# Performance work log

Measured on AMD Instinct MI355X. Metric: run time of the kernel, lower is better.

The kernel has to match this reference:

```python
import jax, jax.numpy as jnp
import numpy as np

D_MODEL = 1024
N_HEADS = 16
HEAD_DIM = D_MODEL // N_HEADS  # 64


def setup_inputs() -> dict:
    key = jax.random.key(0)
    k1, k2, k3 = jax.random.split(key, 3)
    x = jax.random.normal(k1, (2, 2048, D_MODEL), dtype=jnp.float32)
    # nn.Linear(d, 3d, bias=False): store transposed so y = x @ W
    w_qkv = jax.random.normal(k2, (D_MODEL, 3 * D_MODEL), dtype=jnp.float32) * (D_MODEL ** -0.5)
    w_proj = jax.random.normal(k3, (D_MODEL, D_MODEL), dtype=jnp.float32) * (D_MODEL ** -0.5)
    return {"x": x, "w_qkv": w_qkv, "w_proj": w_proj}


def reference(x, w_qkv, w_proj):
    b, n, _ = x.shape
    qkv = x @ w_qkv  # [b, n, 3*d_model]
    # einops 'b n (h d qkv) -> qkv b h n d': qkv axis is innermost of the split
    qkv = qkv.reshape(b, n, N_HEADS, HEAD_DIM, 3)
    q = jnp.moveaxis(qkv[..., 0], 1, 2)  # [b, h, n, d]
    k = jnp.moveaxis(qkv[..., 1], 1, 2)
    v = jnp.moveaxis(qkv[..., 2], 1, 2)
    scale = HEAD_DIM ** -0.5
    scores = jnp.einsum('bhqd,bhkd->bhqk', q, k) * scale  # [b, h, n, n]
    causal = jnp.tril(jnp.ones((n, n), dtype=bool))
    scores = jnp.where(causal[None, None], scores, -jnp.inf)
    attn = jax.nn.softmax(scores, axis=-1)
    out = jnp.einsum('bhqk,bhkd->bhqd', attn, v)  # [b, h, n, d]
    out = jnp.moveaxis(out, 1, 2).reshape(b, n, D_MODEL)  # 'b h n d -> b n (h d)'
    return out @ w_proj
```

## Files before the change

kernel.cpp:

```cpp
#include <hip/hip_runtime.h>
#include <cstdint>
#include <cstddef>

#define D_MODEL 1024
#define N_HEADS 16
#define HEAD_DIM 64
#define SEQ 2048
#define BATCH 2

typedef __attribute__((ext_vector_type(8))) short bf16x8;
typedef __attribute__((ext_vector_type(4))) float f32x4;

__device__ inline unsigned short f2bf(float f) {
    union { float f; unsigned u; } v; v.f = f;
    unsigned r = v.u + 0x7fffu + ((v.u >> 16) & 1u);
    return (unsigned short)(r >> 16);
}

__device__ __forceinline__ void gload_lds16(const unsigned short* g, unsigned short* l) {
    __builtin_amdgcn_global_load_lds(
        (const __attribute__((address_space(1))) unsigned int*)g,
        (__attribute__((address_space(3))) unsigned int*)l, 16, 0, 0);
}

#define WAITCNT_VM4 0x0F74
#define WAITCNT_VM0 0x0F70

__global__ __launch_bounds__(256) void fused_convert_kernel(
    const float* __restrict__ X, unsigned short* __restrict__ Xb,
    const float* __restrict__ Wq, unsigned short* __restrict__ Wqt,
    const float* __restrict__ Wp, unsigned short* __restrict__ Wpt)
{
    const int blk = blockIdx.x;
    const int tid = threadIdx.x;
    __shared__ float t[32][33];

    if (blk < 2048) {
        const int idx = blk * 256 + tid;
        const float4* src = (const float4*)X;
        float4 v0 = src[idx * 2], v1 = src[idx * 2 + 1];
        union { unsigned short u[8]; uint4 v; } o;
        o.u[0] = f2bf(v0.x); o.u[1] = f2bf(v0.y); o.u[2] = f2bf(v0.z); o.u[3] = f2bf(v0.w);
        o.u[4] = f2bf(v1.x); o.u[5] = f2bf(v1.y); o.u[6] = f2bf(v1.z); o.u[7] = f2bf(v1.w);
        ((uint4*)Xb)[idx] = o.v;
    } else if (blk < 5120) {
        const int bb = blk - 2048;
        const int c0 = (bb % 96) * 32, r0 = (bb / 96) * 32;
        const int a = tid & 31, b = tid >> 5;
#pragma unroll
        for (int i = 0; i < 32; i += 8)
            t[b + i][a] = Wq[(size_t)(r0 + b + i) * (3 * D_MODEL) + c0 + a];
        __syncthreads();
#pragma unroll
        for (int i = 0; i < 32; i += 8) {
            const int c = c0 + b + i;
            const int np = (c % 3) * 1024 + c / 3;
            Wqt[(size_t)np * D_MODEL + r0 + a] = f2bf(t[a][b + i]);
        }
    } else {
        const int bb = blk - 5120;
        const int c0 = (bb % 32) * 32, r0 = (bb / 32) * 32;
        const int a = tid & 31, b = tid >> 5;
#pragma unroll
        for (int i = 0; i < 32; i += 8)
            t[b + i][a] = Wp[(size_t)(r0 + b + i) * D_MODEL + c0 + a];
        __syncthreads();
#pragma unroll
        for (int i = 0; i < 32; i += 8)
            Wpt[(size_t)(c0 + b + i) * D_MODEL + r0 + a] = f2bf(t[a][b + i]);
    }
}

__global__ __launch_bounds__(256) void v_transpose(
    const unsigned short* __restrict__ V, unsigned short* __restrict__ Vt)
{
    const int n0 = blockIdx.x * 64;
    const int bh = blockIdx.y;
    __shared__ unsigned short t[64 * 72];
    const int tid = threadIdx.x;
    const uint4* src = (const uint4*)(V + ((size_t)bh * SEQ + n0) * HEAD_DIM);
#pragma unroll
    for (int it = 0; it < 2; it++) {
        const int lin = tid + it * 256;
        const int row = lin >> 3, p = lin & 7;
        ((uint4*)t)[row * 9 + p] = src[lin];
    }
    __syncthreads();
#pragma unroll
    for (int it = 0; it < 2; it++) {
        const int lin = tid + it * 256;
        const int drow = lin >> 3, p = lin & 7;
        union { unsigned short u[8]; uint4 v; } o;
#pragma unroll
        for (int e = 0; e < 8; e++) o.u[e] = t[(p * 8 + e) * 72 + drow];
        ((uint4*)(Vt + ((size_t)bh * HEAD_DIM + drow) * SEQ + n0))[p] = o.v;
    }
}

#define GEMM_PIPE3_BODY(A_, B_, KBASE, NITER)                                  \
    const int tid = threadIdx.x;                                               \
    const int w = tid >> 6, lane = tid & 63;                                   \
    const int l15 = lane & 15, quad = lane >> 4;                               \
    const int wr = w >> 1, wc = w & 1;                                         \
    const int row0 = blockIdx.y * 128, col0 = blockIdx.x * 128;                \
    __shared__ unsigned short As[3][4096];                                     \
    __shared__ unsigned short Bs[3][4096];                                     \
    const f32x4 zero4 = {0.f, 0.f, 0.f, 0.f};                                  \
    f32x4 acc[4][4];                                                           \
    _Pragma("unroll") for (int i = 0; i < 4; i++)                              \
        _Pragma("unroll") for (int j = 0; j < 4; j++) acc[i][j] = zero4;       \
    auto stage_ = [&](int sb_, int kt_) {                                      \
        const int k0 = (KBASE) + kt_ * 32 + quad * 8;                          \
        _Pragma("unroll") for (int i = 0; i < 2; i++) {                        \
            const int f = w * 2 + i;                                           \
            gload_lds16((A_) + (size_t)(row0 + f * 16 + l15) * D_MODEL + k0,   \
                        &As[sb_][f * 512 + lane * 8]);                         \
            gload_lds16((B_) + (size_t)(col0 + f * 16 + l15) * D_MODEL + k0,   \
                        &Bs[sb_][f * 512 + lane * 8]);                         \
        }                                                                      \
    };                                                                         \
    stage_(0, 0);                                                              \
    stage_(1, 1);                                                              \
    int sb = 0;                                                                \
    for (int kt = 0; kt < (NITER); kt++) {                                     \
        if (kt < (NITER) - 1) {                                                \
            __builtin_amdgcn_s_waitcnt(WAITCNT_VM4);                           \
            __builtin_amdgcn_s_barrier();                                      \
            if (kt + 2 < (NITER)) stage_((sb + 2 > 2) ? sb - 1 : sb + 2, kt + 2); \
        } else {                                                               \
            __builtin_amdgcn_s_waitcnt(WAITCNT_VM0);                           \
            __builtin_amdgcn_s_barrier();                                      \
        }                                                                      \
        bf16x8 af[4], bfr[4];                                                  \
        _Pragma("unroll") for (int i = 0; i < 4; i++)                          \
            af[i] = *(const bf16x8*)&As[sb][(wr * 4 + i) * 512 + lane * 8];    \
        _Pragma("unroll") for (int j = 0; j < 4; j++)                          \
            bfr[j] = *(const bf16x8*)&Bs[sb][(wc * 4 + j) * 512 + lane * 8];   \
        _Pragma("unroll") for (int i = 0; i < 4; i++)                          \
            _Pragma("unroll") for (int j = 0; j < 4; j++)                      \
                acc[i][j] = __builtin_amdgcn_mfma_f32_16x16x32_bf16(           \
                    af[i], bfr[j], acc[i][j], 0, 0, 0);                        \
        sb = (sb == 2) ? 0 : sb + 1;                                           \
    }

__global__ __launch_bounds__(256) void gemm_qkv_mfma(
    const unsigned short* __restrict__ A, const unsigned short* __restrict__ B,
    unsigned short* __restrict__ Q, unsigned short* __restrict__ Kq,
    unsigned short* __restrict__ Vb)
{
    GEMM_PIPE3_BODY(A, B, 0, 32)
    const int nbase = col0 + wc * 64;
    const int which = nbase >> 10;
    unsigned short* const dst = (which == 0) ? Q : (which == 1) ? Kq : Vb;
    const float oscale = (which == 0) ? 0.125f : 1.0f;
#pragma unroll
    for (int i = 0; i < 4; i++) {
#pragma unroll
        for (int r = 0; r < 4; r++) {
            const int row = row0 + wr * 64 + i * 16 + quad * 4 + r;
            const int bb = row >> 11, n = row & (SEQ - 1);
#pragma unroll
            for (int j = 0; j < 4; j++) {
                const int idx = (nbase + j * 16 + l15) & 1023;
                const int h = idx >> 6, dd = idx & 63;
                dst[(((size_t)(bb * N_HEADS + h)) * SEQ + n) * HEAD_DIM + dd] =
                    f2bf(acc[i][j][r] * oscale);
            }
        }
    }
}

__global__ __launch_bounds__(256) void gemm_proj_splitk(
    const unsigned short* __restrict__ A, const unsigned short* __restrict__ B,
    float* __restrict__ P)
{
    const int kbase = blockIdx.z * 512;
    GEMM_PIPE3_BODY(A, B, kbase, 16)
    float* const dst = P + (size_t)blockIdx.z * (4096ull * 1024ull);
#pragma unroll
    for (int i = 0; i < 4; i++) {
#pragma unroll
        for (int r = 0; r < 4; r++) {
            const int row = row0 + wr * 64 + i * 16 + quad * 4 + r;
#pragma unroll
            for (int j = 0; j < 4; j++) {
                const int c = col0 + wc * 64 + j * 16 + l15;
                dst[(size_t)row * D_MODEL + c] = acc[i][j][r];
            }
        }
    }
}

__global__ __launch_bounds__(256) void add_out_kernel(
    const float* __restrict__ P, float* __restrict__ out)
{
    const float4* p0 = (const float4*)P;
    const float4* p1 = (const float4*)(P + 4096ull * 1024ull);
    float4* o = (float4*)out;
    const int base = (blockIdx.x * 256 + threadIdx.x) * 4;
#pragma unroll
    for (int j = 0; j < 4; j++) {
        float4 a = p0[base + j], b = p1[base + j];
        float4 r = {a.x + b.x, a.y + b.y, a.z + b.z, a.w + b.w};
        o[base + j] = r;
    }
}

__global__ __launch_bounds__(256) void flash_attn_kernel(
    const unsigned short* __restrict__ Q,
    const unsigned short* __restrict__ K,
    const unsigned short* __restrict__ Vt,
    unsigned short* __restrict__ O)
{
    const int idx = blockIdx.x;
    const int bh = idx & 31;
    const int qt2 = idx >> 5;
    const int hi = qt2 >> 3, lo = qt2 & 7;
    const int qt = (hi == 0) ? lo : (hi == 1) ? 31 - lo : (hi == 2) ? lo + 8 : 23 - lo;

    const int tid = threadIdx.x;
    const int w = tid >> 6, lane = tid & 63;
    const int l15 = lane & 15, quad = lane >> 4;

    __shared__ unsigned short Ks[2][4096];
    __shared__ unsigned short Vs[2][4096];
    __shared__ unsigned short Ps[4][1024];

    bf16x8 qf[2];
    {
        const unsigned short* qrow =
            Q + ((size_t)bh * SEQ + qt * 64 + w * 16 + l15) * HEAD_DIM;
        qf[0] = *(const bf16x8*)(qrow + quad * 8);
        qf[1] = *(const bf16x8*)(qrow + 32 + quad * 8);
    }

    const f32x4 zero4 = {0.f, 0.f, 0.f, 0.f};
    f32x4 o_acc[4] = {zero4, zero4, zero4, zero4};
    float m_i = -1e30f, l_i = 0.f;

    auto stage = [&](int bf, int kt_t) {
        const int key0 = kt_t * 64;
#pragma unroll
        for (int i = 0; i < 2; i++) {
            const int f = w * 2 + i;
            const int ct = f >> 1, kh = f & 1;
            gload_lds16(K + ((size_t)bh * SEQ + key0 + ct * 16 + l15) * HEAD_DIM
                          + kh * 32 + quad * 8,
                        &Ks[bf][f * 512 + lane * 8]);
            gload_lds16(Vt + ((size_t)bh * HEAD_DIM + ct * 16 + l15) * SEQ
                           + key0 + kh * 32 + quad * 8,
                        &Vs[bf][f * 512 + lane * 8]);
        }
    };

    stage(0, 0);
    int buf = 0;

    const int qg = qt * 64 + w * 16 + l15;

    for (int kt = 0; kt <= qt; kt++) {
        __syncthreads();
        if (kt < qt) stage(buf ^ 1, kt + 1);

        f32x4 st[4] = {zero4, zero4, zero4, zero4};
#pragma unroll
        for (int kh = 0; kh < 2; kh++) {
#pragma unroll
            for (int ct = 0; ct < 4; ct++) {
                bf16x8 kf = *(const bf16x8*)&Ks[buf][(ct * 2 + kh) * 512 + lane * 8];
                st[ct] = __builtin_amdgcn_mfma_f32_16x16x32_bf16(kf, qf[kh], st[ct], 0, 0, 0);
            }
        }

        const bool diag = (kt == qt);
        float mt = -1e30f;
#pragma unroll
        for (int ct = 0; ct < 4; ct++) {
#pragma unroll
            for (int r = 0; r < 4; r++) {
                float v = st[ct][r];
                const int kg = kt * 64 + ct * 16 + quad * 4 + r;
                if (diag && kg > qg) v = -1e30f;
                st[ct][r] = v;
                mt = fmaxf(mt, v);
            }
        }
        mt = fmaxf(mt, __shfl_xor(mt, 16));
        mt = fmaxf(mt, __shfl_xor(mt, 32));

        const float mn = fmaxf(m_i, mt);
        const float alpha = __expf(m_i - mn);
        m_i = mn;

        float ls = 0.f;
#pragma unroll
        for (int ct = 0; ct < 4; ct++) {
            union { unsigned short u[4]; uint2 v; } pk;
#pragma unroll
            for (int r = 0; r < 4; r++) {
                float p = __expf(st[ct][r] - mn);
                ls += p;
                pk.u[r] = f2bf(p);
            }
            const int addr = (ct >> 1) * 512 + ((ct & 1) * 2 + (quad >> 1)) * 128
                           + l15 * 8 + (quad & 1) * 4;
            *(uint2*)&Ps[w][addr] = pk.v;
        }
        ls += __shfl_xor(ls, 16);
        ls += __shfl_xor(ls, 32);
        l_i = l_i * alpha + ls;

        float ar[4];
#pragma unroll
        for (int r = 0; r < 4; r++)
            ar[r] = __shfl(alpha, (lane & 48) | (quad * 4 + r));
#pragma unroll
        for (int dt = 0; dt < 4; dt++)
#pragma unroll
            for (int r = 0; r < 4; r++)
                o_acc[dt][r] *= ar[r];

#pragma unroll
        for (int kh = 0; kh < 2; kh++) {
            bf16x8 pa = *(const bf16x8*)&Ps[w][kh * 512 + quad * 128 + l15 * 8];
#pragma unroll
            for (int dt = 0; dt < 4; dt++) {
                bf16x8 vf = *(const bf16x8*)&Vs[buf][(dt * 2 + kh) * 512 + lane * 8];
                o_acc[dt] = __builtin_amdgcn_mfma_f32_16x16x32_bf16(pa, vf, o_acc[dt], 0, 0, 0);
            }
        }
        buf ^= 1;
    }

    const float linv = 1.0f / l_i;
    float lr[4];
#pragma unroll
    for (int r = 0; r < 4; r++)
        lr[r] = __shfl(linv, (lane & 48) | (quad * 4 + r));

    const int b = bh >> 4, h = bh & 15;
#pragma unroll
    for (int r = 0; r < 4; r++) {
        const int q = qt * 64 + w * 16 + quad * 4 + r;
        unsigned short* orow = O + ((size_t)b * SEQ + q) * D_MODEL + h * HEAD_DIM;
#pragma unroll
        for (int dt = 0; dt < 4; dt++)
            orow[dt * 16 + l15] = f2bf(o_acc[dt][r] * lr[r]);
    }
}

extern "C" void kernel_launch(void* const* d_in, const int* in_sizes, int n_in,
                              void* d_out, int out_size, void* d_ws, size_t ws_size,
                              hipStream_t stream) {
    const float* x      = (const float*)d_in[0];
    const float* w_qkv  = (const float*)d_in[1];
    const float* w_proj = (const float*)d_in[2];
    float* out = (float*)d_out;

    unsigned short* Xb  = (unsigned short*)d_ws;
    unsigned short* Wqt = Xb  + (size_t)4 * 1024 * 1024;
    unsigned short* Wpt = Wqt + (size_t)3 * 1024 * 1024;
    unsigned short* Qb  = Wpt + (size_t)1 * 1024 * 1024;
    unsigned short* Kb  = Qb  + (size_t)4 * 1024 * 1024;
    unsigned short* Vb  = Kb  + (size_t)4 * 1024 * 1024;
    unsigned short* Vtb = Vb  + (size_t)4 * 1024 * 1024;
    unsigned short* Ob  = Vtb + (size_t)4 * 1024 * 1024;

    float* Pp = (float*)Qb;

    fused_convert_kernel<<<dim3(6144), 256, 0, stream>>>(
        x, Xb, w_qkv, Wqt, w_proj, Wpt);

    gemm_qkv_mfma<<<dim3(3 * D_MODEL / 128, BATCH * SEQ / 128), 256, 0, stream>>>(
        Xb, Wqt, Qb, Kb, Vb);

    v_transpose<<<dim3(SEQ / 64, BATCH * N_HEADS), 256, 0, stream>>>(Vb, Vtb);

    flash_attn_kernel<<<dim3(SEQ / 64 * BATCH * N_HEADS), 256, 0, stream>>>(
        Qb, Kb, Vtb, Ob);

    gemm_proj_splitk<<<dim3(D_MODEL / 128, BATCH * SEQ / 128, 2), 256, 0, stream>>>(
        Ob, Wpt, Pp);

    add_out_kernel<<<dim3(1024), 256, 0, stream>>>(Pp, out);
}
```

Measured before the change: 222.0 us.

## Use hardware bf16 packing, fold Q scale into weights, lazy softmax rescale, setprio

Replaces software bf16 rounding with the packed v_cvt_pk_bf16_f32 instruction across the conversion, QKV epilogue and attention kernels. Moves the 0.125 Q scale into the weight conversion, so the GEMM epilogue no longer multiplies. The attention loop now skips causal masking on non-diagonal tiles, skips the running-max rescale unless the max grows by more than 8, defers the row-sum shuffle reduction to the end, and raises wave priority around the MFMA blocks. The lazy rescale lets values be exponentiated against a stale max, which holds up to a bounded growth but changes the numerics slightly.

New measurement: 217.2 us. 2.2% less time.

```diff
diff --git a/kernel.cpp b/kernel.cpp
--- a/kernel.cpp
+++ b/kernel.cpp
@@ -17,6 +17,15 @@
     return (unsigned short)(r >> 16);
 }
 
+__device__ __forceinline__ unsigned cvtpk_bf16(float lo, float hi) {
+    unsigned r;
+    asm("v_cvt_pk_bf16_f32 %0, %1, %2" : "=v"(r) : "v"(lo), "v"(hi));
+    return r;
+}
+__device__ __forceinline__ unsigned short f2bf_hw(float f) {
+    return (unsigned short)cvtpk_bf16(f, 0.f);
+}
+
 __device__ __forceinline__ void gload_lds16(const unsigned short* g, unsigned short* l) {
     __builtin_amdgcn_global_load_lds(
         (const __attribute__((address_space(1))) unsigned int*)g,
@@ -39,10 +48,12 @@
         const int idx = blk * 256 + tid;
         const float4* src = (const float4*)X;
         float4 v0 = src[idx * 2], v1 = src[idx * 2 + 1];
-        union { unsigned short u[8]; uint4 v; } o;
-        o.u[0] = f2bf(v0.x); o.u[1] = f2bf(v0.y); o.u[2] = f2bf(v0.z); o.u[3] = f2bf(v0.w);
-        o.u[4] = f2bf(v1.x); o.u[5] = f2bf(v1.y); o.u[6] = f2bf(v1.z); o.u[7] = f2bf(v1.w);
-        ((uint4*)Xb)[idx] = o.v;
+        uint4 o;
+        o.x = cvtpk_bf16(v0.x, v0.y);
+        o.y = cvtpk_bf16(v0.z, v0.w);
+        o.z = cvtpk_bf16(v1.x, v1.y);
+        o.w = cvtpk_bf16(v1.z, v1.w);
+        ((uint4*)Xb)[idx] = o;
     } else if (blk < 5120) {
         const int bb = blk - 2048;
         const int c0 = (bb % 96) * 32, r0 = (bb / 96) * 32;
@@ -54,8 +65,10 @@
 #pragma unroll
         for (int i = 0; i < 32; i += 8) {
             const int c = c0 + b + i;
-            const int np = (c % 3) * 1024 + c / 3;
-            Wqt[(size_t)np * D_MODEL + r0 + a] = f2bf(t[a][b + i]);
+            const int which = c % 3;
+            const int np = which * 1024 + c / 3;
+            const float s = (which == 0) ? 0.125f : 1.0f;
+            Wqt[(size_t)np * D_MODEL + r0 + a] = f2bf_hw(t[a][b + i] * s);
         }
     } else {
         const int bb = blk - 5120;
@@ -67,7 +80,7 @@
         __syncthreads();
 #pragma unroll
         for (int i = 0; i < 32; i += 8)
-            Wpt[(size_t)(c0 + b + i) * D_MODEL + r0 + a] = f2bf(t[a][b + i]);
+            Wpt[(size_t)(c0 + b + i) * D_MODEL + r0 + a] = f2bf_hw(t[a][b + i]);
     }
 }
 
@@ -152,19 +165,21 @@
     const int nbase = col0 + wc * 64;
     const int which = nbase >> 10;
     unsigned short* const dst = (which == 0) ? Q : (which == 1) ? Kq : Vb;
-    const float oscale = (which == 0) ? 0.125f : 1.0f;
 #pragma unroll
     for (int i = 0; i < 4; i++) {
-#pragma unroll
-        for (int r = 0; r < 4; r++) {
-            const int row = row0 + wr * 64 + i * 16 + quad * 4 + r;
-            const int bb = row >> 11, n = row & (SEQ - 1);
+        const int rowb = row0 + wr * 64 + i * 16 + quad * 4;
+        const int bb = rowb >> 11, n = rowb & (SEQ - 1);
+#pragma unroll
+        for (int rp = 0; rp < 2; rp++) {
 #pragma unroll
             for (int j = 0; j < 4; j++) {
+                const unsigned u = cvtpk_bf16(acc[i][j][2 * rp], acc[i][j][2 * rp + 1]);
                 const int idx = (nbase + j * 16 + l15) & 1023;
                 const int h = idx >> 6, dd = idx & 63;
-                dst[(((size_t)(bb * N_HEADS + h)) * SEQ + n) * HEAD_DIM + dd] =
-                    f2bf(acc[i][j][r] * oscale);
+                unsigned short* p =
+                    dst + (((size_t)(bb * N_HEADS + h)) * SEQ + n + 2 * rp) * HEAD_DIM + dd;
+                p[0] = (unsigned short)u;
+                p[HEAD_DIM] = (unsigned short)(u >> 16);
             }
         }
     }
@@ -263,6 +278,7 @@
         if (kt < qt) stage(buf ^ 1, kt + 1);
 
         f32x4 st[4] = {zero4, zero4, zero4, zero4};
+        __builtin_amdgcn_s_setprio(1);
 #pragma unroll
         for (int kh = 0; kh < 2; kh++) {
 #pragma unroll
@@ -271,55 +287,65 @@
                 st[ct] = __builtin_amdgcn_mfma_f32_16x16x32_bf16(kf, qf[kh], st[ct], 0, 0, 0);
             }
         }
-
-        const bool diag = (kt == qt);
+        __builtin_amdgcn_s_setprio(0);
+
         float mt = -1e30f;
-#pragma unroll
-        for (int ct = 0; ct < 4; ct++) {
-#pragma unroll
-            for (int r = 0; r < 4; r++) {
-                float v = st[ct][r];
-                const int kg = kt * 64 + ct * 16 + quad * 4 + r;
-                if (diag && kg > qg) v = -1e30f;
-                st[ct][r] = v;
-                mt = fmaxf(mt, v);
+        if (kt == qt) {
+#pragma unroll
+            for (int ct = 0; ct < 4; ct++) {
+#pragma unroll
+                for (int r = 0; r < 4; r++) {
+                    const int kg = kt * 64 + ct * 16 + quad * 4 + r;
+                    float v = (kg > qg) ? -1e30f : st[ct][r];
+                    st[ct][r] = v;
+                    mt = fmaxf(mt, v);
+                }
             }
+        } else {
+#pragma unroll
+            for (int ct = 0; ct < 4; ct++)
+#pragma unroll
+                for (int r = 0; r < 4; r++)
+                    mt = fmaxf(mt, st[ct][r]);
         }
         mt = fmaxf(mt, __shfl_xor(mt, 16));
         mt = fmaxf(mt, __shfl_xor(mt, 32));
 
-        const float mn = fmaxf(m_i, mt);
-        const float alpha = __expf(m_i - mn);
-        m_i = mn;
+        float mn = m_i;
+        if (!__all(mt <= m_i + 8.0f)) {
+            mn = fmaxf(m_i, mt);
+            const float alpha = __expf(m_i - mn);
+            m_i = mn;
+            l_i *= alpha;
+            float ar[4];
+#pragma unroll
+            for (int r = 0; r < 4; r++)
+                ar[r] = __shfl(alpha, (lane & 48) | (quad * 4 + r));
+#pragma unroll
+            for (int dt = 0; dt < 4; dt++)
+#pragma unroll
+                for (int r = 0; r < 4; r++)
+                    o_acc[dt][r] *= ar[r];
+        }
 
         float ls = 0.f;
 #pragma unroll
         for (int ct = 0; ct < 4; ct++) {
-            union { unsigned short u[4]; uint2 v; } pk;
-#pragma unroll
-            for (int r = 0; r < 4; r++) {
-                float p = __expf(st[ct][r] - mn);
-                ls += p;
-                pk.u[r] = f2bf(p);
-            }
+            const float p0 = __expf(st[ct][0] - mn);
+            const float p1 = __expf(st[ct][1] - mn);
+            const float p2 = __expf(st[ct][2] - mn);
+            const float p3 = __expf(st[ct][3] - mn);
+            ls += (p0 + p1) + (p2 + p3);
+            uint2 pk2;
+            pk2.x = cvtpk_bf16(p0, p1);
+            pk2.y = cvtpk_bf16(p2, p3);
             const int addr = (ct >> 1) * 512 + ((ct & 1) * 2 + (quad >> 1)) * 128
                            + l15 * 8 + (quad & 1) * 4;
-            *(uint2*)&Ps[w][addr] = pk.v;
-        }
-        ls += __shfl_xor(ls, 16);
-        ls += __shfl_xor(ls, 32);
-        l_i = l_i * alpha + ls;
-
-        float ar[4];
-#pragma unroll
-        for (int r = 0; r < 4; r++)
-            ar[r] = __shfl(alpha, (lane & 48) | (quad * 4 + r));
-#pragma unroll
-        for (int dt = 0; dt < 4; dt++)
-#pragma unroll
-            for (int r = 0; r < 4; r++)
-                o_acc[dt][r] *= ar[r];
-
+            *(uint2*)&Ps[w][addr] = pk2;
+        }
+        l_i += ls;
+
+        __builtin_amdgcn_s_setprio(1);
 #pragma unroll
         for (int kh = 0; kh < 2; kh++) {
             bf16x8 pa = *(const bf16x8*)&Ps[w][kh * 512 + quad * 128 + l15 * 8];
@@ -329,9 +355,12 @@
                 o_acc[dt] = __builtin_amdgcn_mfma_f32_16x16x32_bf16(pa, vf, o_acc[dt], 0, 0, 0);
             }
         }
+        __builtin_amdgcn_s_setprio(0);
         buf ^= 1;
     }
 
+    l_i += __shfl_xor(l_i, 16);
+    l_i += __shfl_xor(l_i, 32);
     const float linv = 1.0f / l_i;
     float lr[4];
 #pragma unroll
@@ -345,7 +374,7 @@
         unsigned short* orow = O + ((size_t)b * SEQ + q) * D_MODEL + h * HEAD_DIM;
 #pragma unroll
         for (int dt = 0; dt < 4; dt++)
-            orow[dt * 16 + l15] = f2bf(o_acc[dt][r] * lr[r]);
+            orow[dt * 16 + l15] = f2bf_hw(o_acc[dt][r] * lr[r]);
     }
 }
 
```
